# Performance work log

Measured on AMD Instinct MI355X. Metric: run time of the kernel, lower is better.

## Reference

```python
import jax, jax.numpy as jnp
import numpy as np

N_NODES = 100000
N_EDGES = 500000
DIM = 128
HID = 128

def setup_inputs() -> dict:
    key = jax.random.key(0)
    k1, k2, k3, k4, k5, k6 = jax.random.split(key, 6)
    z = jax.random.normal(k1, (N_NODES, DIM), dtype=jnp.float32)
    edge_index = jax.random.randint(k2, (2, N_EDGES), 0, N_NODES, dtype=jnp.int64)
    # Linear params (torch default init: U(-1/sqrt(fan_in), 1/sqrt(fan_in)))
    b1_lim = 1.0 / np.sqrt(3 * DIM)
    b2_lim = 1.0 / np.sqrt(HID)
    W1 = jax.random.uniform(k3, (3 * DIM, HID), jnp.float32, -b1_lim, b1_lim)
    b1 = jax.random.uniform(k4, (HID,), jnp.float32, -b1_lim, b1_lim)
    W2 = jax.random.uniform(k5, (HID, 1), jnp.float32, -b2_lim, b2_lim)
    b2 = jax.random.uniform(k6, (1,), jnp.float32, -b2_lim, b2_lim)
    return {"z": z, "edge_index": edge_index, "W1": W1, "b1": b1, "W2": W2, "b2": b2}

def reference(z, edge_index, W1, b1, W2, b2):
    u, v = edge_index[0], edge_index[1]
    zu = z[u]                      # [E, dim]
    zv = z[v]                      # [E, dim]
    feat = jnp.concatenate([zu, zv, jnp.abs(zu - zv)], axis=1)  # [E, 3*dim]
    h = jax.nn.relu(feat @ W1 + b1)   # [E, hid]
    logit = h @ W2 + b2               # [E, 1]
    return logit.squeeze(-1)          # [E]
```

## Files before the change

### kernel.cpp

```cpp
#include <hip/hip_runtime.h>
#include <hip/hip_bf16.h>
#include <cstdint>


typedef __bf16 bf16_t;
typedef __bf16 bf16x8 __attribute__((ext_vector_type(8)));
typedef float  floatx4 __attribute__((ext_vector_type(4)));

#define DIM 128
#define LDA 136
#define NB_TILE 64
#define E_TILE 64
#define PACK_BLOCKS 8

__device__ inline float bflo(unsigned w) { return __uint_as_float(w << 16); }
__device__ inline float bfhi(unsigned w) { return __uint_as_float(w & 0xffff0000u); }
__device__ inline float bf2f(unsigned short u) { return __uint_as_float(((unsigned)u) << 16); }

__global__ __launch_bounds__(256)
void precompute_kernel(const float* __restrict__ z,
                       const float* __restrict__ W1,
                       bf16_t* __restrict__ zb,
                       bf16_t* __restrict__ P,
                       bf16_t* __restrict__ Wc,
                       int Nn, int nblk) {
    __shared__ __align__(16) bf16_t A[NB_TILE * LDA];
    const int tid = threadIdx.x;

    if ((int)blockIdx.x >= nblk) {
        int pid = ((int)blockIdx.x - nblk) * 256 + tid;
        int lane = pid & 63;
        int fidx = pid >> 6;
        int nt = fidx & 7, ks = fidx >> 3;
        int n  = nt * 16 + (lane & 15);
        int k0 = ks * 32 + (lane >> 4) * 8;
        bf16x8 o;
#pragma unroll
        for (int j = 0; j < 8; ++j) o[j] = (bf16_t)W1[(256 + k0 + j) * DIM + n];
        reinterpret_cast<bf16x8*>(Wc)[fidx * 64 + lane] = o;
        return;
    }

    const int node0 = (int)blockIdx.x * NB_TILE;
#pragma unroll
    for (int i = 0; i < 4; ++i) {
        int t = i * 256 + tid;
        int m = t >> 4, c = (t & 15) * 8;
        int node = node0 + m;
        int nc = node < Nn ? node : Nn - 1;
        const float4* src = reinterpret_cast<const float4*>(z + (size_t)nc * DIM + c);
        float4 a = src[0], b = src[1];
        bf16x8 o;
        o[0]=(bf16_t)a.x; o[1]=(bf16_t)a.y; o[2]=(bf16_t)a.z; o[3]=(bf16_t)a.w;
        o[4]=(bf16_t)b.x; o[5]=(bf16_t)b.y; o[6]=(bf16_t)b.z; o[7]=(bf16_t)b.w;
        *reinterpret_cast<bf16x8*>(&A[m * LDA + c]) = o;
        if (node < Nn)
            *reinterpret_cast<bf16x8*>(zb + (size_t)node * DIM + c) = o;
    }
    __syncthreads();

    const int wave = tid >> 6, lane = tid & 63;
    const int l15 = lane & 15, quad = lane >> 4;

    floatx4 acc[4][4];
#pragma unroll
    for (int mt = 0; mt < 4; ++mt)
#pragma unroll
        for (int nt = 0; nt < 4; ++nt) acc[mt][nt] = (floatx4)0.0f;

#pragma unroll
    for (int ks = 0; ks < 4; ++ks) {
        bf16x8 bfrag[4];
#pragma unroll
        for (int nt = 0; nt < 4; ++nt) {
            int np = wave * 64 + nt * 16 + l15;
            int k0 = ks * 32 + quad * 8;
            const float* wsrc = (np < DIM) ? &W1[(size_t)k0 * DIM + np]
                                           : &W1[(size_t)(DIM + k0) * DIM + (np - DIM)];
#pragma unroll
            for (int j = 0; j < 8; ++j) bfrag[nt][j] = (bf16_t)wsrc[(size_t)j * DIM];
        }
#pragma unroll
        for (int mt = 0; mt < 4; ++mt) {
            bf16x8 afrag = *reinterpret_cast<const bf16x8*>(
                &A[(mt * 16 + l15) * LDA + ks * 32 + quad * 8]);
#pragma unroll
            for (int nt = 0; nt < 4; ++nt)
                acc[mt][nt] = __builtin_amdgcn_mfma_f32_16x16x32_bf16(
                    afrag, bfrag[nt], acc[mt][nt], 0, 0, 0);
        }
    }

#pragma unroll
    for (int mt = 0; mt < 4; ++mt)
#pragma unroll
        for (int r = 0; r < 4; ++r) {
            int node = node0 + mt * 16 + quad * 4 + r;
            if (node < Nn) {
#pragma unroll
                for (int nt = 0; nt < 4; ++nt) {
                    int np = wave * 64 + nt * 16 + l15;
                    P[(size_t)node * 256 + np] = (bf16_t)acc[mt][nt][r];
                }
            }
        }
}

__global__ __launch_bounds__(256)
void edge_kernel(const bf16_t* __restrict__ zb,
                 const bf16_t* __restrict__ P,
                 const bf16_t* __restrict__ Wc,
                 const int* __restrict__ ei,
                 const float* __restrict__ b1,
                 const float* __restrict__ W2,
                 const float* __restrict__ b2,
                 float* __restrict__ out, int E) {
    __shared__ __align__(16) bf16_t A[E_TILE * LDA];
    __shared__ __align__(16) bf16_t H[E_TILE * LDA];
    __shared__ float red[4][E_TILE];

    const int tid = threadIdx.x;
    const int ebase = (int)blockIdx.x * E_TILE;

#pragma unroll
    for (int i = 0; i < 4; ++i) {
        int t = i * 256 + tid;
        int m = t >> 4, c = (t & 15) * 8;
        int e = ebase + m; if (e >= E) e = E - 1;
        int u = ei[e], v = ei[E + e];
        uint4 zu = *reinterpret_cast<const uint4*>(zb + (size_t)u * DIM + c);
        uint4 zv = *reinterpret_cast<const uint4*>(zb + (size_t)v * DIM + c);
        uint4 pa = *reinterpret_cast<const uint4*>(P + (size_t)u * 256 + c);
        uint4 pb = *reinterpret_cast<const uint4*>(P + (size_t)v * 256 + DIM + c);
        bf16x8 d, h;
        d[0]=(bf16_t)fabsf(bflo(zu.x)-bflo(zv.x));
        d[1]=(bf16_t)fabsf(bfhi(zu.x)-bfhi(zv.x));
        d[2]=(bf16_t)fabsf(bflo(zu.y)-bflo(zv.y));
        d[3]=(bf16_t)fabsf(bfhi(zu.y)-bfhi(zv.y));
        d[4]=(bf16_t)fabsf(bflo(zu.z)-bflo(zv.z));
        d[5]=(bf16_t)fabsf(bfhi(zu.z)-bfhi(zv.z));
        d[6]=(bf16_t)fabsf(bflo(zu.w)-bflo(zv.w));
        d[7]=(bf16_t)fabsf(bfhi(zu.w)-bfhi(zv.w));
        h[0]=(bf16_t)(bflo(pa.x)+bflo(pb.x));
        h[1]=(bf16_t)(bfhi(pa.x)+bfhi(pb.x));
        h[2]=(bf16_t)(bflo(pa.y)+bflo(pb.y));
        h[3]=(bf16_t)(bfhi(pa.y)+bfhi(pb.y));
        h[4]=(bf16_t)(bflo(pa.z)+bflo(pb.z));
        h[5]=(bf16_t)(bfhi(pa.z)+bfhi(pb.z));
        h[6]=(bf16_t)(bflo(pa.w)+bflo(pb.w));
        h[7]=(bf16_t)(bfhi(pa.w)+bfhi(pb.w));
        *reinterpret_cast<bf16x8*>(&A[m * LDA + c]) = d;
        *reinterpret_cast<bf16x8*>(&H[m * LDA + c]) = h;
    }
    __syncthreads();

    const int wave = tid >> 6, lane = tid & 63;
    const int l15 = lane & 15, quad = lane >> 4;

    float b1v[2], w2v[2];
#pragma unroll
    for (int nt = 0; nt < 2; ++nt) {
        int n = (wave * 2 + nt) * 16 + l15;
        b1v[nt] = b1[n];
        w2v[nt] = W2[n];
    }

    floatx4 acc[4][2];
#pragma unroll
    for (int mt = 0; mt < 4; ++mt)
#pragma unroll
        for (int nt = 0; nt < 2; ++nt) acc[mt][nt] = (floatx4)0.0f;

    const bf16x8* WcF = reinterpret_cast<const bf16x8*>(Wc);
#pragma unroll
    for (int ks = 0; ks < 4; ++ks) {
        bf16x8 bfrag[2];
#pragma unroll
        for (int nt = 0; nt < 2; ++nt)
            bfrag[nt] = WcF[(ks * 8 + wave * 2 + nt) * 64 + lane];
#pragma unroll
        for (int mt = 0; mt < 4; ++mt) {
            bf16x8 afrag = *reinterpret_cast<const bf16x8*>(
                &A[(mt * 16 + l15) * LDA + ks * 32 + quad * 8]);
#pragma unroll
            for (int nt = 0; nt < 2; ++nt)
                acc[mt][nt] = __builtin_amdgcn_mfma_f32_16x16x32_bf16(
                    afrag, bfrag[nt], acc[mt][nt], 0, 0, 0);
        }
    }

    const unsigned short* Hs = reinterpret_cast<const unsigned short*>(H);
#pragma unroll
    for (int mt = 0; mt < 4; ++mt)
#pragma unroll
        for (int r = 0; r < 4; ++r) {
            int m = mt * 16 + quad * 4 + r;
            float s = 0.f;
#pragma unroll
            for (int nt = 0; nt < 2; ++nt) {
                int n = (wave * 2 + nt) * 16 + l15;
                float h = acc[mt][nt][r] + b1v[nt] + bf2f(Hs[m * LDA + n]);
                h = fmaxf(h, 0.f);
                s += h * w2v[nt];
            }
            s += __shfl_xor(s, 1);
            s += __shfl_xor(s, 2);
            s += __shfl_xor(s, 4);
            s += __shfl_xor(s, 8);
            if (l15 == 0) red[wave][m] = s;
        }
    __syncthreads();

    if (tid < E_TILE) {
        int e = ebase + tid;
        if (e < E) out[e] = red[0][tid] + red[1][tid] + red[2][tid] + red[3][tid] + b2[0];
    }
}

#define K3 384
#define ROW_ELEMS 392
#define N_KSTEP 12
#define N_NTILE 8

__global__ void pack_w1_kernel(const float* __restrict__ W1, bf16_t* __restrict__ Wp) {
    int f = blockIdx.x * 256 + threadIdx.x;
    if (f >= N_KSTEP * N_NTILE * 64) return;
    int lane = f & 63;
    int nt   = (f >> 6) & 7;
    int ks   = f >> 9;
    int n  = nt * 16 + (lane & 15);
    int k0 = ks * 32 + (lane >> 4) * 8;
    bf16x8 o;
#pragma unroll
    for (int j = 0; j < 8; ++j) o[j] = (bf16_t)W1[(k0 + j) * DIM + n];
    reinterpret_cast<bf16x8*>(Wp)[f] = o;
}

__global__ __launch_bounds__(256)
void decode_fallback(const float* __restrict__ zsrc,
                     const int* __restrict__ ei,
                     const bf16_t* __restrict__ Wp,
                     const float* __restrict__ b1,
                     const float* __restrict__ W2,
                     const float* __restrict__ b2,
                     float* __restrict__ out, int E) {
    __shared__ __align__(16) bf16_t Atile[E_TILE * ROW_ELEMS];
    __shared__ float red[2][E_TILE];
    const int tid = threadIdx.x;
    const int ebase = blockIdx.x * E_TILE;
#pragma unroll
    for (int i = 0; i < 8; ++i) {
        int half  = i * 16 + (tid >> 4);
        int m     = half >> 1;
        int which = half & 1;
        int e = ebase + m; if (e >= E) e = E - 1;
        int node = ei[which * E + e];
        int l16 = tid & 15;
        bf16_t* dst = &Atile[m * ROW_ELEMS + which * DIM + l16 * 8];
        const float4* src = reinterpret_cast<const float4*>(
            zsrc + (size_t)node * DIM + l16 * 8);
        float4 a = src[0], b = src[1];
        bf16x8 o;
        o[0]=(bf16_t)a.x; o[1]=(bf16_t)a.y; o[2]=(bf16_t)a.z; o[3]=(bf16_t)a.w;
        o[4]=(bf16_t)b.x; o[5]=(bf16_t)b.y; o[6]=(bf16_t)b.z; o[7]=(bf16_t)b.w;
        *reinterpret_cast<bf16x8*>(dst) = o;
    }
    __syncthreads();
#pragma unroll
    for (int i = 0; i < 4; ++i) {
        int chunk = i * 256 + tid;
        int m  = chunk >> 4;
        int cc = (chunk & 15) * 8;
        uint4 au = *reinterpret_cast<const uint4*>(&Atile[m * ROW_ELEMS + cc]);
        uint4 av = *reinterpret_cast<const uint4*>(&Atile[m * ROW_ELEMS + DIM + cc]);
        bf16x8 d;
        d[0]=(bf16_t)fabsf(bflo(au.x)-bflo(av.x));
        d[1]=(bf16_t)fabsf(bfhi(au.x)-bfhi(av.x));
        d[2]=(bf16_t)fabsf(bflo(au.y)-bflo(av.y));
        d[3]=(bf16_t)fabsf(bfhi(au.y)-bfhi(av.y));
        d[4]=(bf16_t)fabsf(bflo(au.z)-bflo(av.z));
        d[5]=(bf16_t)fabsf(bfhi(au.z)-bfhi(av.z));
        d[6]=(bf16_t)fabsf(bflo(au.w)-bflo(av.w));
        d[7]=(bf16_t)fabsf(bfhi(au.w)-bfhi(av.w));
        *reinterpret_cast<bf16x8*>(&Atile[m * ROW_ELEMS + 2 * DIM + cc]) = d;
    }
    __syncthreads();
    const int wave = tid >> 6, lane = tid & 63;
    const int wm = wave >> 1, wn = wave & 1;
    const int l15 = lane & 15, quad = lane >> 4;
    floatx4 acc[2][4];
#pragma unroll
    for (int mt = 0; mt < 2; ++mt)
#pragma unroll
        for (int nt = 0; nt < 4; ++nt) acc[mt][nt] = (floatx4)0.0f;
    float b1v[4], w2v[4];
#pragma unroll
    for (int nt = 0; nt < 4; ++nt) {
        int n = (wn * 4 + nt) * 16 + l15;
        b1v[nt] = b1[n];
        w2v[nt] = W2[n];
    }
    const bf16x8* WpF = reinterpret_cast<const bf16x8*>(Wp);
#pragma unroll
    for (int ks = 0; ks < N_KSTEP; ++ks) {
        bf16x8 bfrag[4];
#pragma unroll
        for (int nt = 0; nt < 4; ++nt)
            bfrag[nt] = WpF[(ks * N_NTILE + wn * 4 + nt) * 64 + lane];
#pragma unroll
        for (int mt = 0; mt < 2; ++mt) {
            int m = wm * 32 + mt * 16 + l15;
            bf16x8 afrag = *reinterpret_cast<const bf16x8*>(
                &Atile[m * ROW_ELEMS + ks * 32 + quad * 8]);
#pragma unroll
            for (int nt = 0; nt < 4; ++nt)
                acc[mt][nt] = __builtin_amdgcn_mfma_f32_16x16x32_bf16(
                    afrag, bfrag[nt], acc[mt][nt], 0, 0, 0);
        }
    }
    float partial[2][4];
#pragma unroll
    for (int mt = 0; mt < 2; ++mt)
#pragma unroll
        for (int r = 0; r < 4; ++r) {
            float s = 0.f;
#pragma unroll
            for (int nt = 0; nt < 4; ++nt) {
                float h = acc[mt][nt][r] + b1v[nt];
                h = fmaxf(h, 0.f);
                s += h * w2v[nt];
            }
            s += __shfl_xor(s, 1);
            s += __shfl_xor(s, 2);
            s += __shfl_xor(s, 4);
            s += __shfl_xor(s, 8);
            partial[mt][r] = s;
        }
    if (l15 == 0) {
#pragma unroll
        for (int mt = 0; mt < 2; ++mt)
#pragma unroll
            for (int r = 0; r < 4; ++r) {
                int m = wm * 32 + mt * 16 + quad * 4 + r;
                red[wn][m] = partial[mt][r];
            }
    }
    __syncthreads();
    if (tid < E_TILE) {
        int e = ebase + tid;
        if (e < E) out[e] = red[0][tid] + red[1][tid] + b2[0];
    }
}

extern "C" void kernel_launch(void* const* d_in, const int* in_sizes, int n_in,
                              void* d_out, int out_size, void* d_ws, size_t ws_size,
                              hipStream_t stream) {
    const float* z  = (const float*)d_in[0];
    const int*   ei = (const int*)d_in[1];
    const float* W1 = (const float*)d_in[2];
    const float* b1 = (const float*)d_in[3];
    const float* W2 = (const float*)d_in[4];
    const float* b2 = (const float*)d_in[5];
    float* out = (float*)d_out;

    const int E  = in_sizes[1] / 2;
    const int Nn = in_sizes[0] / DIM;

    const size_t zb_bytes = (size_t)Nn * DIM * sizeof(bf16_t);
    const size_t p_bytes  = (size_t)Nn * 256 * sizeof(bf16_t);
    const size_t wc_bytes = 4 * 8 * 64 * 16;

    const int eblocks = (E + E_TILE - 1) / E_TILE;

    if (ws_size >= zb_bytes + p_bytes + wc_bytes) {
        bf16_t* zb = (bf16_t*)d_ws;
        bf16_t* P  = (bf16_t*)((char*)d_ws + zb_bytes);
        bf16_t* Wc = (bf16_t*)((char*)d_ws + zb_bytes + p_bytes);
        const int nblk = (Nn + NB_TILE - 1) / NB_TILE;
        hipLaunchKernelGGL(precompute_kernel, dim3(nblk + PACK_BLOCKS), dim3(256),
                           0, stream, z, W1, zb, P, Wc, Nn, nblk);
        hipLaunchKernelGGL(edge_kernel, dim3(eblocks), dim3(256), 0, stream,
                           zb, P, Wc, ei, b1, W2, b2, out, E);
    } else {
        bf16_t* wp = (bf16_t*)d_ws;
        hipLaunchKernelGGL(pack_w1_kernel, dim3((N_KSTEP * N_NTILE * 64 + 255) / 256),
                           dim3(256), 0, stream, W1, wp);
        hipLaunchKernelGGL(decode_fallback, dim3(eblocks), dim3(256), 0, stream,
                           z, ei, wp, b1, W2, b2, out, E);
    }
}
```

Before: 205.9 us.

## Pre-pack all W1 fragments once and batch edge gathers for memory-level parallelism

A separate pack kernel now converts all of W1 into bf16 MFMA fragment layout. The node precompute kernel reads these packed fragments directly instead of doing strided fp32 loads and conversions in every block. The edge kernel loads all indices first, then issues every zb and P gather before doing any arithmetic, so more loads are in flight at once. It also adds a launch_bounds occupancy hint. The cost is one extra kernel launch and higher register pressure from holding 16 uint4 values per thread.

New measurement: 197.5 us. 1.04x faster.

```diff
diff --git a/kernel.cpp b/kernel.cpp
--- a/kernel.cpp
+++ b/kernel.cpp
@@ -11,37 +11,37 @@
 #define LDA 136
 #define NB_TILE 64
 #define E_TILE 64
-#define PACK_BLOCKS 8
+#define N_KSTEP 12
+#define N_NTILE 8
 
 __device__ inline float bflo(unsigned w) { return __uint_as_float(w << 16); }
 __device__ inline float bfhi(unsigned w) { return __uint_as_float(w & 0xffff0000u); }
 __device__ inline float bf2f(unsigned short u) { return __uint_as_float(((unsigned)u) << 16); }
 
+__global__ void pack_w1_kernel(const float* __restrict__ W1, bf16_t* __restrict__ Wp) {
+    int f = blockIdx.x * 256 + threadIdx.x;
+    if (f >= N_KSTEP * N_NTILE * 64) return;
+    int lane = f & 63;
+    int nt   = (f >> 6) & 7;
+    int ks   = f >> 9;
+    int n  = nt * 16 + (lane & 15);
+    int k0 = ks * 32 + (lane >> 4) * 8;
+    bf16x8 o;
+#pragma unroll
+    for (int j = 0; j < 8; ++j) o[j] = (bf16_t)W1[(k0 + j) * DIM + n];
+    reinterpret_cast<bf16x8*>(Wp)[f] = o;
+}
+
 __global__ __launch_bounds__(256)
 void precompute_kernel(const float* __restrict__ z,
-                       const float* __restrict__ W1,
+                       const bf16_t* __restrict__ Wp,
                        bf16_t* __restrict__ zb,
                        bf16_t* __restrict__ P,
-                       bf16_t* __restrict__ Wc,
-                       int Nn, int nblk) {
+                       int Nn) {
     __shared__ __align__(16) bf16_t A[NB_TILE * LDA];
     const int tid = threadIdx.x;
-
-    if ((int)blockIdx.x >= nblk) {
-        int pid = ((int)blockIdx.x - nblk) * 256 + tid;
-        int lane = pid & 63;
-        int fidx = pid >> 6;
-        int nt = fidx & 7, ks = fidx >> 3;
-        int n  = nt * 16 + (lane & 15);
-        int k0 = ks * 32 + (lane >> 4) * 8;
-        bf16x8 o;
-#pragma unroll
-        for (int j = 0; j < 8; ++j) o[j] = (bf16_t)W1[(256 + k0 + j) * DIM + n];
-        reinterpret_cast<bf16x8*>(Wc)[fidx * 64 + lane] = o;
-        return;
-    }
-
     const int node0 = (int)blockIdx.x * NB_TILE;
+
 #pragma unroll
     for (int i = 0; i < 4; ++i) {
         int t = i * 256 + tid;
@@ -61,6 +61,7 @@
 
     const int wave = tid >> 6, lane = tid & 63;
     const int l15 = lane & 15, quad = lane >> 4;
+    const bf16x8* WpF = reinterpret_cast<const bf16x8*>(Wp);
 
     floatx4 acc[4][4];
 #pragma unroll
@@ -73,12 +74,8 @@
         bf16x8 bfrag[4];
 #pragma unroll
         for (int nt = 0; nt < 4; ++nt) {
-            int np = wave * 64 + nt * 16 + l15;
-            int k0 = ks * 32 + quad * 8;
-            const float* wsrc = (np < DIM) ? &W1[(size_t)k0 * DIM + np]
-                                           : &W1[(size_t)(DIM + k0) * DIM + (np - DIM)];
-#pragma unroll
-            for (int j = 0; j < 8; ++j) bfrag[nt][j] = (bf16_t)wsrc[(size_t)j * DIM];
+            int f = (ks + (wave >> 1) * 4) * 8 + (wave & 1) * 4 + nt;
+            bfrag[nt] = WpF[f * 64 + lane];
         }
 #pragma unroll
         for (int mt = 0; mt < 4; ++mt) {
@@ -106,10 +103,10 @@
         }
 }
 
-__global__ __launch_bounds__(256)
+__global__ __launch_bounds__(256, 4)
 void edge_kernel(const bf16_t* __restrict__ zb,
                  const bf16_t* __restrict__ P,
-                 const bf16_t* __restrict__ Wc,
+                 const bf16_t* __restrict__ Wp,
                  const int* __restrict__ ei,
                  const float* __restrict__ b1,
                  const float* __restrict__ W2,
@@ -121,18 +118,32 @@
 
     const int tid = threadIdx.x;
     const int ebase = (int)blockIdx.x * E_TILE;
-
-#pragma unroll
-    for (int i = 0; i < 4; ++i) {
-        int t = i * 256 + tid;
-        int m = t >> 4, c = (t & 15) * 8;
-        int e = ebase + m; if (e >= E) e = E - 1;
-        int u = ei[e], v = ei[E + e];
-        uint4 zu = *reinterpret_cast<const uint4*>(zb + (size_t)u * DIM + c);
-        uint4 zv = *reinterpret_cast<const uint4*>(zb + (size_t)v * DIM + c);
-        uint4 pa = *reinterpret_cast<const uint4*>(P + (size_t)u * 256 + c);
-        uint4 pb = *reinterpret_cast<const uint4*>(P + (size_t)v * 256 + DIM + c);
-        bf16x8 d, h;
+    const int r0 = tid >> 4;
+    const int c  = (tid & 15) * 8;
+
+    int uu[4], vv[4];
+#pragma unroll
+    for (int i = 0; i < 4; ++i) {
+        int e = ebase + i * 16 + r0; if (e >= E) e = E - 1;
+        uu[i] = ei[e];
+        vv[i] = ei[E + e];
+    }
+    uint4 gzu[4], gzv[4], gpa[4], gpb[4];
+#pragma unroll
+    for (int i = 0; i < 4; ++i) {
+        gzu[i] = *reinterpret_cast<const uint4*>(zb + (size_t)uu[i] * DIM + c);
+        gzv[i] = *reinterpret_cast<const uint4*>(zb + (size_t)vv[i] * DIM + c);
+    }
+#pragma unroll
+    for (int i = 0; i < 4; ++i) {
+        gpa[i] = *reinterpret_cast<const uint4*>(P + (size_t)uu[i] * 256 + c);
+        gpb[i] = *reinterpret_cast<const uint4*>(P + (size_t)vv[i] * 256 + DIM + c);
+    }
+#pragma unroll
+    for (int i = 0; i < 4; ++i) {
+        int m = i * 16 + r0;
+        uint4 zu = gzu[i], zv = gzv[i];
+        bf16x8 d;
         d[0]=(bf16_t)fabsf(bflo(zu.x)-bflo(zv.x));
         d[1]=(bf16_t)fabsf(bfhi(zu.x)-bfhi(zv.x));
         d[2]=(bf16_t)fabsf(bflo(zu.y)-bflo(zv.y));
@@ -141,6 +152,13 @@
         d[5]=(bf16_t)fabsf(bfhi(zu.z)-bfhi(zv.z));
         d[6]=(bf16_t)fabsf(bflo(zu.w)-bflo(zv.w));
         d[7]=(bf16_t)fabsf(bfhi(zu.w)-bfhi(zv.w));
+        *reinterpret_cast<bf16x8*>(&A[m * LDA + c]) = d;
+    }
+#pragma unroll
+    for (int i = 0; i < 4; ++i) {
+        int m = i * 16 + r0;
+        uint4 pa = gpa[i], pb = gpb[i];
+        bf16x8 h;
         h[0]=(bf16_t)(bflo(pa.x)+bflo(pb.x));
         h[1]=(bf16_t)(bfhi(pa.x)+bfhi(pb.x));
         h[2]=(bf16_t)(bflo(pa.y)+bflo(pb.y));
@@ -149,7 +167,6 @@
         h[5]=(bf16_t)(bfhi(pa.z)+bfhi(pb.z));
         h[6]=(bf16_t)(bflo(pa.w)+bflo(pb.w));
         h[7]=(bf16_t)(bfhi(pa.w)+bfhi(pb.w));
-        *reinterpret_cast<bf16x8*>(&A[m * LDA + c]) = d;
         *reinterpret_cast<bf16x8*>(&H[m * LDA + c]) = h;
     }
     __syncthreads();
@@ -171,13 +188,13 @@
 #pragma unroll
         for (int nt = 0; nt < 2; ++nt) acc[mt][nt] = (floatx4)0.0f;
 
-    const bf16x8* WcF = reinterpret_cast<const bf16x8*>(Wc);
+    const bf16x8* WpF = reinterpret_cast<const bf16x8*>(Wp);
 #pragma unroll
     for (int ks = 0; ks < 4; ++ks) {
         bf16x8 bfrag[2];
 #pragma unroll
         for (int nt = 0; nt < 2; ++nt)
-            bfrag[nt] = WcF[(ks * 8 + wave * 2 + nt) * 64 + lane];
+            bfrag[nt] = WpF[((ks + 8) * 8 + wave * 2 + nt) * 64 + lane];
 #pragma unroll
         for (int mt = 0; mt < 4; ++mt) {
             bf16x8 afrag = *reinterpret_cast<const bf16x8*>(
@@ -217,24 +234,7 @@
     }
 }
 
-#define K3 384
 #define ROW_ELEMS 392
-#define N_KSTEP 12
-#define N_NTILE 8
-
-__global__ void pack_w1_kernel(const float* __restrict__ W1, bf16_t* __restrict__ Wp) {
-    int f = blockIdx.x * 256 + threadIdx.x;
-    if (f >= N_KSTEP * N_NTILE * 64) return;
-    int lane = f & 63;
-    int nt   = (f >> 6) & 7;
-    int ks   = f >> 9;
-    int n  = nt * 16 + (lane & 15);
-    int k0 = ks * 32 + (lane >> 4) * 8;
-    bf16x8 o;
-#pragma unroll
-    for (int j = 0; j < 8; ++j) o[j] = (bf16_t)W1[(k0 + j) * DIM + n];
-    reinterpret_cast<bf16x8*>(Wp)[f] = o;
-}
 
 __global__ __launch_bounds__(256)
 void decode_fallback(const float* __restrict__ zsrc,
@@ -366,25 +366,25 @@
     const int E  = in_sizes[1] / 2;
     const int Nn = in_sizes[0] / DIM;
 
+    const size_t wp_bytes = (size_t)N_KSTEP * N_NTILE * 64 * 16;
     const size_t zb_bytes = (size_t)Nn * DIM * sizeof(bf16_t);
     const size_t p_bytes  = (size_t)Nn * 256 * sizeof(bf16_t);
-    const size_t wc_bytes = 4 * 8 * 64 * 16;
 
     const int eblocks = (E + E_TILE - 1) / E_TILE;
-
-    if (ws_size >= zb_bytes + p_bytes + wc_bytes) {
-        bf16_t* zb = (bf16_t*)d_ws;
-        bf16_t* P  = (bf16_t*)((char*)d_ws + zb_bytes);
-        bf16_t* Wc = (bf16_t*)((char*)d_ws + zb_bytes + p_bytes);
+    const int packblk = (N_KSTEP * N_NTILE * 64 + 255) / 256;
+
+    bf16_t* wp = (bf16_t*)d_ws;
+    hipLaunchKernelGGL(pack_w1_kernel, dim3(packblk), dim3(256), 0, stream, W1, wp);
+
+    if (ws_size >= wp_bytes + zb_bytes + p_bytes) {
+        bf16_t* zb = (bf16_t*)((char*)d_ws + wp_bytes);
+        bf16_t* P  = (bf16_t*)((char*)d_ws + wp_bytes + zb_bytes);
         const int nblk = (Nn + NB_TILE - 1) / NB_TILE;
-        hipLaunchKernelGGL(precompute_kernel, dim3(nblk + PACK_BLOCKS), dim3(256),
-                           0, stream, z, W1, zb, P, Wc, Nn, nblk);
+        hipLaunchKernelGGL(precompute_kernel, dim3(nblk), dim3(256), 0, stream,
+                           z, wp, zb, P, Nn);
         hipLaunchKernelGGL(edge_kernel, dim3(eblocks), dim3(256), 0, stream,
-                           zb, P, Wc, ei, b1, W2, b2, out, E);
+                           zb, P, wp, ei, b1, W2, b2, out, E);
     } else {
-        bf16_t* wp = (bf16_t*)d_ws;
-        hipLaunchKernelGGL(pack_w1_kernel, dim3((N_KSTEP * N_NTILE * 64 + 255) / 256),
-                           dim3(256), 0, stream, W1, wp);
         hipLaunchKernelGGL(decode_fallback, dim3(eblocks), dim3(256), 0, stream,
                            z, ei, wp, b1, W2, b2, out, E);
     }
```
